# Kernel tuning notes

Measured on AMD Instinct MI355X. Metric: run time of the kernel, lower is better.

Reference implementation:

```python
import jax, jax.numpy as jnp
import numpy as np

N = 50000; E = 800000; F_IN = 128; H = 16; G = 256
DIMS = [F_IN, H, 2 * H, 4 * H, 4 * H, 8 * H]
EPS = 1e-5


def setup_inputs() -> dict:
    key = jax.random.key(0)
    ks = iter(jax.random.split(key, 40))
    inp = {}
    inp["x"] = jax.random.normal(next(ks), (N, F_IN), dtype=jnp.float32)
    inp["edge_index"] = jax.random.randint(next(ks), (2, E), 0, N, dtype=jnp.int32)
    inp["edge_weight"] = jax.random.uniform(next(ks), (E,), dtype=jnp.float32)
    inp["batch"] = jnp.sort(jax.random.randint(next(ks), (N,), 0, G, dtype=jnp.int32))
    for i in range(5):
        din, dout = DIMS[i], DIMS[i + 1]
        inp[f"W{i+1}"] = jax.random.normal(next(ks), (din, dout), dtype=jnp.float32) / np.sqrt(din).astype(np.float32)
        inp[f"b{i+1}"] = jnp.zeros((dout,), jnp.float32)
        inp[f"g{i+1}"] = jnp.ones((dout,), jnp.float32)
        inp[f"bt{i+1}"] = jnp.zeros((dout,), jnp.float32)
    inp["fc1_w"] = jax.random.normal(next(ks), (8 * H, 4 * H), dtype=jnp.float32) / np.sqrt(8 * H).astype(np.float32)
    inp["fc1_b"] = jnp.zeros((4 * H,), jnp.float32)
    inp["fc2_w"] = jax.random.normal(next(ks), (4 * H, 1), dtype=jnp.float32) / np.sqrt(4 * H).astype(np.float32)
    inp["fc2_b"] = jnp.zeros((1,), jnp.float32)
    return inp


def _gcn_norm(edge_index, edge_weight, n):
    # PyG GCNConv: add self-loops (weight 1), symmetric deg^-1/2 normalization.
    loop = jnp.arange(n, dtype=edge_index.dtype)
    row = jnp.concatenate([edge_index[0], loop])  # source
    col = jnp.concatenate([edge_index[1], loop])  # target
    w = jnp.concatenate([edge_weight, jnp.ones((n,), edge_weight.dtype)])
    deg = jax.ops.segment_sum(w, col, num_segments=n)
    dis = jnp.where(deg > 0, jax.lax.rsqrt(jnp.maximum(deg, 1e-12)), 0.0)
    return row, col, dis[row] * w * dis[col]


def _bn(h, g, b):
    # BatchNorm1d, training-mode batch statistics (biased variance, eps=1e-5)
    mu = h.mean(0)
    v = h.var(0)
    return g * (h - mu) * jax.lax.rsqrt(v + EPS) + b


def reference(x, edge_index, edge_weight, batch,
              W1, b1, g1, bt1, W2, b2, g2, bt2, W3, b3, g3, bt3,
              W4, b4, g4, bt4, W5, b5, g5, bt5,
              fc1_w, fc1_b, fc2_w, fc2_b):
    n = x.shape[0]
    row, col, norm = _gcn_norm(edge_index, edge_weight, n)

    def conv(h, W, b):
        m = h @ W                                   # [N, dout] dense transform
        agg = jax.ops.segment_sum(m[row] * norm[:, None], col, num_segments=n)
        return agg + b

    h = _bn(jax.nn.relu(conv(x, W1, b1)), g1, bt1)
    h = _bn(jax.nn.relu(conv(h, W2, b2)), g2, bt2)
    h = _bn(jax.nn.relu(conv(h, W3, b3)), g3, bt3)
    h = jax.nn.relu(_bn(conv(h, W4, b4), g4, bt4))   # layer4: conv->bn->relu
    h = _bn(conv(h, W5, b5), g5, bt5)                # layer5: conv->bn
    pooled = jax.ops.segment_sum(h, batch, num_segments=G)  # global_add_pool -> [G, 8H]
    p = jax.nn.relu(pooled)
    p = jax.nn.relu(p @ fc1_w + fc1_b)
    # dropout is identity in eval mode
    return (p @ fc2_w + fc2_b).reshape(-1)          # [G]
```

## Files before the change

kernel.cpp:

```cpp
#include <hip/hip_runtime.h>
#include <stdint.h>

#define NN 50000
#define NE 800000
#define NG 256
#define NBUCKET 16
#define PARTSZ (NBUCKET * 256)

#define NBKT 391
#define ABLK 391
#define ASLICE 2048
#define BCAP 2560

#define AFF4(u, sc, sh) { u.x = fmaxf(sc.x*u.x+sh.x,0.f); u.y = fmaxf(sc.y*u.y+sh.y,0.f); \
                          u.z = fmaxf(sc.z*u.z+sh.z,0.f); u.w = fmaxf(sc.w*u.w+sh.w,0.f); }

__device__ __forceinline__ void bn_coef(const double* __restrict__ partIn,
                                        const float* __restrict__ gmv,
                                        const float* __restrict__ btv,
                                        int tid, int n, float* scs, float* shs) {
    double s = 0., q = 0.;
#pragma unroll
    for (int b2 = 0; b2 < NBUCKET; ++b2) {
        s += partIn[b2 * 256 + tid];
        q += partIn[b2 * 256 + 128 + tid];
    }
    double mu = s / (double)n;
    double var = q / (double)n - mu * mu;
    float a = gmv[tid] * rsqrtf((float)var + 1e-5f);
    scs[tid] = a;
    shs[tid] = btv[tid] - (float)mu * a;
}

__device__ __forceinline__ void scan_totals(const int* __restrict__ totals,
                                            int* __restrict__ sbase, int tid) {
    if (tid < 64) {
        const int C = (NBKT + 63) / 64;
        int tv[C];
        int s = 0;
        int i0 = tid * C;
#pragma unroll
        for (int j = 0; j < C; ++j) {
            int idx = i0 + j;
            int x = (idx < NBKT) ? totals[idx] : 0;
            tv[j] = x; s += x;
        }
        int inc = s;
        for (int off = 1; off < 64; off <<= 1) {
            int t2 = __shfl_up(inc, off, 64);
            if (tid >= off) inc += t2;
        }
        int run = inc - s;
#pragma unroll
        for (int j = 0; j < C; ++j) {
            int idx = i0 + j;
            if (idx < NBKT) sbase[idx] = run;
            run += tv[j];
        }
        if (tid == 63) sbase[NBKT] = run;
    }
}

__global__ void kA1(const int* __restrict__ col, int* __restrict__ bb,
                    double* __restrict__ zz, int zn, int e) {
    __shared__ int cnt[NBKT];
    for (int j = threadIdx.x; j < NBKT; j += 256) cnt[j] = 0;
    for (int i = blockIdx.x * 256 + threadIdx.x; i < zn; i += ABLK * 256) zz[i] = 0.;
    __syncthreads();
    int start = blockIdx.x * ASLICE;
    int end = min(start + ASLICE, e);
    for (int i = start + threadIdx.x; i < end; i += 256)
        atomicAdd(&cnt[col[i] >> 7], 1);
    __syncthreads();
    for (int j = threadIdx.x; j < NBKT; j += 256) bb[blockIdx.x * NBKT + j] = cnt[j];
}

__global__ void kA2a(int* __restrict__ bb, int* __restrict__ totals) {
    __shared__ int v[ABLK];
    int k = blockIdx.x;
    int tid = threadIdx.x;
    for (int b = tid; b < ABLK; b += 256) v[b] = bb[b * NBKT + k];
    __syncthreads();
    if (tid < 64) {
        const int C = (ABLK + 63) / 64;
        int tv[C];
        int s = 0;
        int i0 = tid * C;
#pragma unroll
        for (int j = 0; j < C; ++j) {
            int idx = i0 + j;
            int x = (idx < ABLK) ? v[idx] : 0;
            tv[j] = x; s += x;
        }
        int inc = s;
        for (int off = 1; off < 64; off <<= 1) {
            int t2 = __shfl_up(inc, off, 64);
            if (tid >= off) inc += t2;
        }
        int run = inc - s;
#pragma unroll
        for (int j = 0; j < C; ++j) {
            int idx = i0 + j;
            if (idx < ABLK) v[idx] = run;
            run += tv[j];
        }
        if (tid == 63) totals[k] = run;
    }
    __syncthreads();
    for (int b = tid; b < ABLK; b += 256) bb[b * NBKT + k] = v[b];
}

__global__ void kA3g(const int* __restrict__ row, const int* __restrict__ col,
                     const float* __restrict__ ew, const int* __restrict__ bb,
                     const int* __restrict__ totals, int2* __restrict__ staging,
                     const float* __restrict__ x, const float* __restrict__ W0,
                     float* __restrict__ m1, int e, int n) {
    __shared__ int cur[NBKT];
    __shared__ int sbase[NBKT + 1];
    __shared__ float Wl[128 * 16];
    int tid = threadIdx.x;
    if ((int)blockIdx.x < ABLK) {
        scan_totals(totals, sbase, tid);
        __syncthreads();
        for (int j = tid; j < NBKT; j += 256)
            cur[j] = sbase[j] + bb[blockIdx.x * NBKT + j];
        __syncthreads();
        int start = blockIdx.x * ASLICE;
        int end = min(start + ASLICE, e);
        for (int i = start + tid; i < end; i += 256) {
            int c = col[i];
            int p = atomicAdd(&cur[c >> 7], 1);
            staging[p] = make_int2(row[i] | ((c & 127) << 16), __float_as_int(ew[i]));
        }
        return;
    }
    int bid = (int)blockIdx.x - ABLK;
    for (int i = tid; i < 128 * 16 / 4; i += 256)
        ((float4*)Wl)[i] = ((const float4*)W0)[i];
    __syncthreads();
    int jq = tid % 4, group = tid / 4;
    int node0 = (bid * 64 + group) * 2;
    const float4* h4 = (const float4*)x;
    int hb[2]; bool val[2];
#pragma unroll
    for (int i = 0; i < 2; ++i) {
        int nd = node0 + i;
        val[i] = nd < n;
        hb[i] = (val[i] ? nd : n - 1) * 32;
    }
    float4 acc[2];
    acc[0] = {0,0,0,0}; acc[1] = {0,0,0,0};
#pragma unroll 4
    for (int k4 = 0; k4 < 32; ++k4) {
        const float* wb = &Wl[(k4 * 4) * 16 + jq * 4];
        float4 w0 = *(const float4*)(wb);
        float4 w1 = *(const float4*)(wb + 16);
        float4 w2 = *(const float4*)(wb + 32);
        float4 w3 = *(const float4*)(wb + 48);
#pragma unroll
        for (int i = 0; i < 2; ++i) {
            float4 hv = h4[hb[i] + k4];
            acc[i].x += hv.x*w0.x + hv.y*w1.x + hv.z*w2.x + hv.w*w3.x;
            acc[i].y += hv.x*w0.y + hv.y*w1.y + hv.z*w2.y + hv.w*w3.y;
            acc[i].z += hv.x*w0.z + hv.y*w1.z + hv.z*w2.z + hv.w*w3.z;
            acc[i].w += hv.x*w0.w + hv.y*w1.w + hv.z*w2.w + hv.w*w3.w;
        }
    }
#pragma unroll
    for (int i = 0; i < 2; ++i)
        if (val[i]) ((float4*)m1)[(node0 + i) * 4 + jq] = acc[i];
}

__global__ void __launch_bounds__(256) kB(const int* __restrict__ totals,
                                          const int2* __restrict__ staging,
                                          int2* __restrict__ csr, int* __restrict__ ptr,
                                          float* __restrict__ dis, int n) {
    __shared__ int2 st[BCAP];
    __shared__ int2 outb[BCAP];
    __shared__ int hist[129];
    __shared__ int cur[128];
    __shared__ int sbase[NBKT + 1];
    int k = blockIdx.x, t = threadIdx.x;
    scan_totals(totals, sbase, t);
    if (t < 129) hist[t] = 0;
    __syncthreads();
    int base = sbase[k], cnt = sbase[k + 1] - sbase[k];
    int node0 = k << 7;
    int ncov = min(128, n - node0);
    if (cnt <= BCAP) {
        for (int i = t; i < cnt; i += 256) {
            int2 v = staging[base + i];
            st[i] = v;
            atomicAdd(&hist[v.x >> 16], 1);
        }
        __syncthreads();
        if (t == 0) {
            int run = 0;
            for (int j = 0; j < 128; ++j) { int h = hist[j]; hist[j] = run; run += h; }
            hist[128] = run;
        }
        __syncthreads();
        if (t < 128) cur[t] = hist[t];
        if (t < ncov) ptr[node0 + t] = base + hist[t];
        __syncthreads();
        for (int i = t; i < cnt; i += 256) {
            int2 v = st[i];
            int j = v.x >> 16;
            int p = atomicAdd(&cur[j], 1);
            outb[p] = make_int2(v.x & 0xFFFF, v.y);
        }
        __syncthreads();
        for (int i = t; i < cnt; i += 256) csr[base + i] = outb[i];
        if (t < ncov) {
            double s = 1.;
            int a = hist[t], b2 = hist[t + 1];
            for (int p = a; p < b2; ++p) s += (double)__int_as_float(outb[p].y);
            dis[node0 + t] = rsqrtf((float)s);
        }
    } else {
        for (int i = t; i < cnt; i += 256) atomicAdd(&hist[staging[base + i].x >> 16], 1);
        __syncthreads();
        if (t == 0) {
            int run = 0;
            for (int j = 0; j < 128; ++j) { int h = hist[j]; hist[j] = run; run += h; }
            hist[128] = run;
        }
        __syncthreads();
        if (t < 128) cur[t] = hist[t];
        if (t < ncov) ptr[node0 + t] = base + hist[t];
        __syncthreads();
        for (int i = t; i < cnt; i += 256) {
            int2 v = staging[base + i];
            int j = v.x >> 16;
            int p = atomicAdd(&cur[j], 1);
            csr[base + p] = make_int2(v.x & 0xFFFF, v.y);
        }
        __threadfence_block();
        __syncthreads();
        if (t < ncov) {
            double s = 1.;
            int a = hist[t], b2 = hist[t + 1];
            for (int p = a; p < b2; ++p) s += (double)__int_as_float(csr[base + p].y);
            dis[node0 + t] = rsqrtf((float)s);
        }
    }
    if (k == gridDim.x - 1 && t == 0) ptr[n] = sbase[NBKT];
}

__global__ void k_l1gather(const float* __restrict__ src, const int* __restrict__ ptr,
                           int2* __restrict__ csr, const float* __restrict__ dis,
                           const float* __restrict__ bias, double* __restrict__ partOut,
                           float* __restrict__ out, int n) {
    int tid = threadIdx.x;
    int t = blockIdx.x * 256 + tid;
    int node = t >> 2;
    int l4 = t & 3;
    bool valid = node < n;
    int nc = valid ? node : n - 1;
    const float4* s4 = (const float4*)src;
    float dc = dis[nc];
    float w0 = dc * dc;
    float4 v = s4[nc * 4 + l4];
    double ax = (double)(w0 * v.x), ay = (double)(w0 * v.y);
    double az = (double)(w0 * v.z), aw = (double)(w0 * v.w);
    int p0 = ptr[nc], p1 = ptr[nc + 1];
    int p = p0;
    for (; p + 4 <= p1; p += 4) {
        int2 c0 = csr[p], c1 = csr[p+1], c2 = csr[p+2], c3 = csr[p+3];
        float e0 = dis[c0.x] * __int_as_float(c0.y) * dc;
        float e1 = dis[c1.x] * __int_as_float(c1.y) * dc;
        float e2 = dis[c2.x] * __int_as_float(c2.y) * dc;
        float e3 = dis[c3.x] * __int_as_float(c3.y) * dc;
        float4 u0 = s4[c0.x * 4 + l4];
        float4 u1 = s4[c1.x * 4 + l4];
        float4 u2 = s4[c2.x * 4 + l4];
        float4 u3 = s4[c3.x * 4 + l4];
        ax += (double)(e0*u0.x) + (double)(e1*u1.x) + (double)(e2*u2.x) + (double)(e3*u3.x);
        ay += (double)(e0*u0.y) + (double)(e1*u1.y) + (double)(e2*u2.y) + (double)(e3*u3.y);
        az += (double)(e0*u0.z) + (double)(e1*u1.z) + (double)(e2*u2.z) + (double)(e3*u3.z);
        aw += (double)(e0*u0.w) + (double)(e1*u1.w) + (double)(e2*u2.w) + (double)(e3*u3.w);
        if (l4 == 0) {
            csr[p]   = make_int2(c0.x, __float_as_int(e0));
            csr[p+1] = make_int2(c1.x, __float_as_int(e1));
            csr[p+2] = make_int2(c2.x, __float_as_int(e2));
            csr[p+3] = make_int2(c3.x, __float_as_int(e3));
        }
    }
    for (; p < p1; ++p) {
        int2 ce = csr[p];
        float w = dis[ce.x] * __int_as_float(ce.y) * dc;
        float4 u = s4[ce.x * 4 + l4];
        ax += (double)(w*u.x); ay += (double)(w*u.y);
        az += (double)(w*u.z); aw += (double)(w*u.w);
        if (l4 == 0) csr[p] = make_int2(ce.x, __float_as_int(w));
    }
    float4 b = ((const float4*)bias)[l4];
    float4 acc;
    acc.x = fmaxf((float)ax + b.x, 0.f);
    acc.y = fmaxf((float)ay + b.y, 0.f);
    acc.z = fmaxf((float)az + b.z, 0.f);
    acc.w = fmaxf((float)aw + b.w, 0.f);
    if (valid) ((float4*)out)[nc * 4 + l4] = acc;
    float s0 = valid ? acc.x : 0.f, s1 = valid ? acc.y : 0.f;
    float s2 = valid ? acc.z : 0.f, s3 = valid ? acc.w : 0.f;
    float q0 = s0*s0, q1 = s1*s1, q2 = s2*s2, q3 = s3*s3;
    for (int off = 4; off < 64; off <<= 1) {
        s0 += __shfl_down(s0, off, 64); s1 += __shfl_down(s1, off, 64);
        s2 += __shfl_down(s2, off, 64); s3 += __shfl_down(s3, off, 64);
        q0 += __shfl_down(q0, off, 64); q1 += __shfl_down(q1, off, 64);
        q2 += __shfl_down(q2, off, 64); q3 += __shfl_down(q3, off, 64);
    }
    int lane = tid & 63;
    int bkt = (blockIdx.x & (NBUCKET - 1)) * 256;
    if (lane < 4) {
        atomicAdd(&partOut[bkt + 4*lane + 0], (double)s0);
        atomicAdd(&partOut[bkt + 4*lane + 1], (double)s1);
        atomicAdd(&partOut[bkt + 4*lane + 2], (double)s2);
        atomicAdd(&partOut[bkt + 4*lane + 3], (double)s3);
        atomicAdd(&partOut[bkt + 128 + 4*lane + 0], (double)q0);
        atomicAdd(&partOut[bkt + 128 + 4*lane + 1], (double)q1);
        atomicAdd(&partOut[bkt + 128 + 4*lane + 2], (double)q2);
        atomicAdd(&partOut[bkt + 128 + 4*lane + 3], (double)q3);
    }
}

template <int DIN, int DOUT, int EP, int POSTAFF, int RELU, int NPB>
__global__ void __launch_bounds__(256) k_fused(
        const float* __restrict__ src, const int* __restrict__ ptr,
        const int2* __restrict__ csr, const float* __restrict__ dis,
        const double* __restrict__ partIn, const float* __restrict__ gmv,
        const float* __restrict__ btv, const float* __restrict__ W,
        const float* __restrict__ bias, double* __restrict__ partOut,
        float* __restrict__ out, int n) {
    const int TPN1 = DIN / 4, LPN = TPN1 * EP, GN1 = 256 / LPN;
    const int TPN2 = DOUT / 4, G2 = 256 / TPN2;
    const int HS = DIN + 4;
    __shared__ float Wl[DIN * DOUT];
    __shared__ float hrow[NPB * HS];
    __shared__ float scs[DIN], shs[DIN];
    __shared__ double ls[DOUT], lq[DOUT];
    int tid = threadIdx.x;
    for (int i = tid; i < DIN * DOUT / 4; i += 256)
        ((float4*)Wl)[i] = ((const float4*)W)[i];
    if (tid < DIN) bn_coef(partIn, gmv, btv, tid, n, scs, shs);
    if (tid < DOUT) { ls[tid] = 0.; lq[tid] = 0.; }
    __syncthreads();

    int nodebase = blockIdx.x * NPB;
    {
        int grp = tid / LPN, r = tid % LPN;
        int e0 = r / TPN1, l4 = r % TPN1;
        float4 sc = ((const float4*)scs)[l4];
        float4 sh = ((const float4*)shs)[l4];
        const float4* s4 = (const float4*)src;
#pragma unroll
        for (int pass = 0; pass < NPB / GN1; ++pass) {
            int nl = pass * GN1 + grp;
            int node = nodebase + nl;
            int nc = node < n ? node : n - 1;
            double ax = 0., ay = 0., az = 0., aw = 0.;
            double sumw = 0.;
            if (e0 == 0) {
                float d = dis[nc];
                float w0 = d * d;
                float4 v = s4[(size_t)nc * TPN1 + l4];
                ax = (double)(w0*v.x); ay = (double)(w0*v.y);
                az = (double)(w0*v.z); aw = (double)(w0*v.w);
                sumw = (double)w0;
            }
            int p0 = ptr[nc], p1 = ptr[nc + 1];
            int p = p0 + e0;
            for (; p + 3 * EP < p1; p += 4 * EP) {
                int2 c0 = csr[p], c1 = csr[p + EP], c2 = csr[p + 2*EP], c3 = csr[p + 3*EP];
                float e0w = __int_as_float(c0.y), e1w = __int_as_float(c1.y);
                float e2w = __int_as_float(c2.y), e3w = __int_as_float(c3.y);
                float4 u0 = s4[(size_t)c0.x * TPN1 + l4];
                float4 u1 = s4[(size_t)c1.x * TPN1 + l4];
                float4 u2 = s4[(size_t)c2.x * TPN1 + l4];
                float4 u3 = s4[(size_t)c3.x * TPN1 + l4];
                ax += (double)(e0w*u0.x) + (double)(e1w*u1.x) + (double)(e2w*u2.x) + (double)(e3w*u3.x);
                ay += (double)(e0w*u0.y) + (double)(e1w*u1.y) + (double)(e2w*u2.y) + (double)(e3w*u3.y);
                az += (double)(e0w*u0.z) + (double)(e1w*u1.z) + (double)(e2w*u2.z) + (double)(e3w*u3.z);
                aw += (double)(e0w*u0.w) + (double)(e1w*u1.w) + (double)(e2w*u2.w) + (double)(e3w*u3.w);
                if (POSTAFF) sumw += (double)e0w + (double)e1w + (double)e2w + (double)e3w;
            }
            for (; p < p1; p += EP) {
                int2 ce = csr[p];
                float w = __int_as_float(ce.y);
                float4 u = s4[(size_t)ce.x * TPN1 + l4];
                ax += (double)(w*u.x); ay += (double)(w*u.y);
                az += (double)(w*u.z); aw += (double)(w*u.w);
                if (POSTAFF) sumw += (double)w;
            }
#pragma unroll
            for (int off = TPN1; off < LPN; off <<= 1) {
                ax += __shfl_xor(ax, off, 64);
                ay += __shfl_xor(ay, off, 64);
                az += __shfl_xor(az, off, 64);
                aw += __shfl_xor(aw, off, 64);
                if (POSTAFF) sumw += __shfl_xor(sumw, off, 64);
            }
            if (e0 == 0) {
                float4 acc;
                float sw = (float)sumw;
                acc.x = sc.x * (float)ax + sh.x * sw;
                acc.y = sc.y * (float)ay + sh.y * sw;
                acc.z = sc.z * (float)az + sh.z * sw;
                acc.w = sc.w * (float)aw + sh.w * sw;
                *(float4*)&hrow[nl * HS + (l4 << 2)] = acc;
            }
        }
    }
    __syncthreads();
    {
        int jq = tid % TPN2, g2 = tid / TPN2;
        float4 bv = ((const float4*)bias)[jq];
        float4 sv = {0,0,0,0}, qv = {0,0,0,0};
        for (int nl = g2; nl < NPB; nl += G2) {
            int node = nodebase + nl;
            bool valid = node < n;
            float4 a = {0.f, 0.f, 0.f, 0.f};
#pragma unroll
            for (int k4 = 0; k4 < DIN / 4; ++k4) {
                float4 hv = *(const float4*)&hrow[nl * HS + (k4 << 2)];
                const float* wb = &Wl[(k4 * 4) * DOUT + jq * 4];
                float4 w0 = *(const float4*)(wb);
                float4 w1 = *(const float4*)(wb + DOUT);
                float4 w2 = *(const float4*)(wb + 2 * DOUT);
                float4 w3 = *(const float4*)(wb + 3 * DOUT);
                a.x += hv.x*w0.x + hv.y*w1.x + hv.z*w2.x + hv.w*w3.x;
                a.y += hv.x*w0.y + hv.y*w1.y + hv.z*w2.y + hv.w*w3.y;
                a.z += hv.x*w0.z + hv.y*w1.z + hv.z*w2.z + hv.w*w3.z;
                a.w += hv.x*w0.w + hv.y*w1.w + hv.z*w2.w + hv.w*w3.w;
            }
            a.x += bv.x; a.y += bv.y; a.z += bv.z; a.w += bv.w;
            if (RELU) {
                a.x = fmaxf(a.x, 0.f); a.y = fmaxf(a.y, 0.f);
                a.z = fmaxf(a.z, 0.f); a.w = fmaxf(a.w, 0.f);
            }
            if (valid) {
                ((float4*)out)[(size_t)node * TPN2 + jq] = a;
                sv.x += a.x; sv.y += a.y; sv.z += a.z; sv.w += a.w;
                qv.x += a.x*a.x; qv.y += a.y*a.y; qv.z += a.z*a.z; qv.w += a.w*a.w;
            }
        }
        for (int off = TPN2; off < 64; off <<= 1) {
            sv.x += __shfl_down(sv.x, off, 64); sv.y += __shfl_down(sv.y, off, 64);
            sv.z += __shfl_down(sv.z, off, 64); sv.w += __shfl_down(sv.w, off, 64);
            qv.x += __shfl_down(qv.x, off, 64); qv.y += __shfl_down(qv.y, off, 64);
            qv.z += __shfl_down(qv.z, off, 64); qv.w += __shfl_down(qv.w, off, 64);
        }
        int lane = tid & 63;
        if (lane < TPN2) {
            atomicAdd(&ls[4*lane+0], (double)sv.x); atomicAdd(&ls[4*lane+1], (double)sv.y);
            atomicAdd(&ls[4*lane+2], (double)sv.z); atomicAdd(&ls[4*lane+3], (double)sv.w);
            atomicAdd(&lq[4*lane+0], (double)qv.x); atomicAdd(&lq[4*lane+1], (double)qv.y);
            atomicAdd(&lq[4*lane+2], (double)qv.z); atomicAdd(&lq[4*lane+3], (double)qv.w);
        }
        __syncthreads();
        int bkt = (blockIdx.x & (NBUCKET - 1)) * 256;
        if (tid < DOUT) {
            atomicAdd(&partOut[bkt + tid], ls[tid]);
            atomicAdd(&partOut[bkt + 128 + tid], lq[tid]);
        }
    }
}

template <int D, int POSTAFF, int PREAFF>
__global__ void __launch_bounds__(256) k_wgather(
        const float* __restrict__ src, const int* __restrict__ ptr,
        const int2* __restrict__ csr, const float* __restrict__ dis,
        const double* __restrict__ partIn, const float* __restrict__ gmv,
        const float* __restrict__ btv, float* __restrict__ out, int n) {
    const int RL = D / 4;
    const int EP = 4;
    const int LPN = RL * EP;
    __shared__ float scs[D], shs[D];
    int tid = threadIdx.x;
    if (tid < D) bn_coef(partIn, gmv, btv, tid, n, scs, shs);
    __syncthreads();
    int t = blockIdx.x * 256 + tid;
    int node = t / LPN;
    int r = t - node * LPN;
    int e0 = r / RL;
    int l4 = r - e0 * RL;
    bool valid = node < n;
    int nc = valid ? node : n - 1;
    const float4* s4 = (const float4*)src;
    float4 sc = ((const float4*)scs)[l4], sh = ((const float4*)shs)[l4];
    double ax = 0., ay = 0., az = 0., aw = 0.;
    double sumw = 0.;
    if (e0 == 0) {
        float d = dis[nc];
        float w0 = d * d;
        float4 v = s4[(size_t)nc * RL + l4];
        if (PREAFF) AFF4(v, sc, sh);
        ax = (double)(w0*v.x); ay = (double)(w0*v.y);
        az = (double)(w0*v.z); aw = (double)(w0*v.w);
        sumw = (double)w0;
    }
    int p0 = ptr[nc], p1 = ptr[nc + 1];
    int p = p0 + e0;
    for (; p + 3 * EP < p1; p += 4 * EP) {
        int2 c0 = csr[p], c1 = csr[p + EP], c2 = csr[p + 2*EP], c3 = csr[p + 3*EP];
        float w0 = __int_as_float(c0.y), w1 = __int_as_float(c1.y);
        float w2 = __int_as_float(c2.y), w3 = __int_as_float(c3.y);
        float4 u0 = s4[(size_t)c0.x * RL + l4];
        float4 u1 = s4[(size_t)c1.x * RL + l4];
        float4 u2 = s4[(size_t)c2.x * RL + l4];
        float4 u3 = s4[(size_t)c3.x * RL + l4];
        if (PREAFF) { AFF4(u0, sc, sh); AFF4(u1, sc, sh); AFF4(u2, sc, sh); AFF4(u3, sc, sh); }
        ax += (double)(w0*u0.x) + (double)(w1*u1.x) + (double)(w2*u2.x) + (double)(w3*u3.x);
        ay += (double)(w0*u0.y) + (double)(w1*u1.y) + (double)(w2*u2.y) + (double)(w3*u3.y);
        az += (double)(w0*u0.z) + (double)(w1*u1.z) + (double)(w2*u2.z) + (double)(w3*u3.z);
        aw += (double)(w0*u0.w) + (double)(w1*u1.w) + (double)(w2*u2.w) + (double)(w3*u3.w);
        if (POSTAFF) sumw += (double)w0 + (double)w1 + (double)w2 + (double)w3;
    }
    for (; p < p1; p += EP) {
        int2 ce = csr[p];
        float w = __int_as_float(ce.y);
        float4 u = s4[(size_t)ce.x * RL + l4];
        if (PREAFF) AFF4(u, sc, sh);
        ax += (double)(w*u.x); ay += (double)(w*u.y);
        az += (double)(w*u.z); aw += (double)(w*u.w);
        if (POSTAFF) sumw += (double)w;
    }
#pragma unroll
    for (int off = RL; off < LPN; off <<= 1) {
        ax += __shfl_xor(ax, off, 64); ay += __shfl_xor(ay, off, 64);
        az += __shfl_xor(az, off, 64); aw += __shfl_xor(aw, off, 64);
        if (POSTAFF) sumw += __shfl_xor(sumw, off, 64);
    }
    if (valid && e0 == 0) {
        float4 acc;
        if (POSTAFF) {
            float sw = (float)sumw;
            acc.x = sc.x * (float)ax + sh.x * sw;
            acc.y = sc.y * (float)ay + sh.y * sw;
            acc.z = sc.z * (float)az + sh.z * sw;
            acc.w = sc.w * (float)aw + sh.w * sw;
        } else {
            acc.x = (float)ax; acc.y = (float)ay;
            acc.z = (float)az; acc.w = (float)aw;
        }
        ((float4*)out)[(size_t)nc * RL + l4] = acc;
    }
}

template <int DIN, int DOUT, int RELU, int POOL>
__global__ void k_sgemm(const float* __restrict__ h, const float* __restrict__ W,
                        const float* __restrict__ bias, double* __restrict__ partOut,
                        float* __restrict__ m, const int* __restrict__ batch,
                        double* __restrict__ pooled, int n) {
    const int TPN = DOUT / 4, GPB = 256 / TPN, NPT = 4;
    const int NPBLK = GPB * NPT;
    const int MAXG = 34;
    __shared__ float Wl[DIN * DOUT];
    __shared__ double ls[DOUT], lq[DOUT];
    __shared__ double pool_l[POOL ? MAXG * DOUT : 1];
    __shared__ int gmaxs;
    int tid = threadIdx.x;
    for (int i = tid; i < DIN * DOUT / 4; i += 256)
        ((float4*)Wl)[i] = ((const float4*)W)[i];
    if (tid < DOUT) { ls[tid] = 0.; lq[tid] = 0.; }
    int gbase = 0;
    if (POOL) {
        for (int i = tid; i < MAXG * DOUT; i += 256) pool_l[i] = 0.;
        if (tid == 0) gmaxs = 0;
        int bn0 = blockIdx.x * NPBLK;
        gbase = batch[bn0 < n ? bn0 : n - 1];
    }
    __syncthreads();

    int jq = tid % TPN;
    int group = tid / TPN;
    int node0 = (blockIdx.x * GPB + group) * NPT;
    const float4* h4 = (const float4*)h;
    int hb[NPT]; bool val[NPT];
#pragma unroll
    for (int i = 0; i < NPT; ++i) {
        int nd = node0 + i;
        val[i] = nd < n;
        hb[i] = (val[i] ? nd : n - 1) * (DIN / 4);
    }
    float4 acc[NPT];
#pragma unroll
    for (int i = 0; i < NPT; ++i) acc[i] = {0.f, 0.f, 0.f, 0.f};
#pragma unroll 4
    for (int k4 = 0; k4 < DIN / 4; ++k4) {
        const float* wb = &Wl[(k4 * 4) * DOUT + jq * 4];
        float4 w0 = *(const float4*)(wb);
        float4 w1 = *(const float4*)(wb + DOUT);
        float4 w2 = *(const float4*)(wb + 2 * DOUT);
        float4 w3 = *(const float4*)(wb + 3 * DOUT);
#pragma unroll
        for (int i = 0; i < NPT; ++i) {
            float4 hv = h4[hb[i] + k4];
            acc[i].x += hv.x*w0.x + hv.y*w1.x + hv.z*w2.x + hv.w*w3.x;
            acc[i].y += hv.x*w0.y + hv.y*w1.y + hv.z*w2.y + hv.w*w3.y;
            acc[i].z += hv.x*w0.z + hv.y*w1.z + hv.z*w2.z + hv.w*w3.z;
            acc[i].w += hv.x*w0.w + hv.y*w1.w + hv.z*w2.w + hv.w*w3.w;
        }
    }
    float4 bv = ((const float4*)bias)[jq];
    float4 sv = {0,0,0,0}, qv = {0,0,0,0};
#pragma unroll
    for (int i = 0; i < NPT; ++i) {
        float4 a = acc[i];
        a.x += bv.x; a.y += bv.y; a.z += bv.z; a.w += bv.w;
        if (RELU) {
            a.x = fmaxf(a.x, 0.f); a.y = fmaxf(a.y, 0.f);
            a.z = fmaxf(a.z, 0.f); a.w = fmaxf(a.w, 0.f);
        }
        if (val[i]) {
            if (POOL) {
                int off = batch[node0 + i] - gbase;
                if (off < MAXG) {
                    atomicAdd(&pool_l[off * DOUT + jq * 4 + 0], (double)a.x);
                    atomicAdd(&pool_l[off * DOUT + jq * 4 + 1], (double)a.y);
                    atomicAdd(&pool_l[off * DOUT + jq * 4 + 2], (double)a.z);
                    atomicAdd(&pool_l[off * DOUT + jq * 4 + 3], (double)a.w);
                    if (jq == 0) atomicMax(&gmaxs, off);
                } else {
                    double* pg = &pooled[(size_t)(gbase + off) * DOUT + jq * 4];
                    atomicAdd(pg + 0, (double)a.x); atomicAdd(pg + 1, (double)a.y);
                    atomicAdd(pg + 2, (double)a.z); atomicAdd(pg + 3, (double)a.w);
                }
            } else {
                ((float4*)m)[(size_t)(node0 + i) * TPN + jq] = a;
            }
            sv.x += a.x; sv.y += a.y; sv.z += a.z; sv.w += a.w;
            qv.x += a.x*a.x; qv.y += a.y*a.y; qv.z += a.z*a.z; qv.w += a.w*a.w;
        }
    }
    for (int off = TPN; off < 64; off <<= 1) {
        sv.x += __shfl_down(sv.x, off, 64); sv.y += __shfl_down(sv.y, off, 64);
        sv.z += __shfl_down(sv.z, off, 64); sv.w += __shfl_down(sv.w, off, 64);
        qv.x += __shfl_down(qv.x, off, 64); qv.y += __shfl_down(qv.y, off, 64);
        qv.z += __shfl_down(qv.z, off, 64); qv.w += __shfl_down(qv.w, off, 64);
    }
    int lane = tid & 63;
    if (lane < TPN) {
        atomicAdd(&ls[4*lane+0], (double)sv.x); atomicAdd(&ls[4*lane+1], (double)sv.y);
        atomicAdd(&ls[4*lane+2], (double)sv.z); atomicAdd(&ls[4*lane+3], (double)sv.w);
        atomicAdd(&lq[4*lane+0], (double)qv.x); atomicAdd(&lq[4*lane+1], (double)qv.y);
        atomicAdd(&lq[4*lane+2], (double)qv.z); atomicAdd(&lq[4*lane+3], (double)qv.w);
    }
    __syncthreads();
    int bkt = (blockIdx.x & (NBUCKET - 1)) * 256;
    if (tid < DOUT) {
        atomicAdd(&partOut[bkt + tid], ls[tid]);
        atomicAdd(&partOut[bkt + 128 + tid], lq[tid]);
    }
    if (POOL) {
        int gm = gmaxs;
        for (int i = tid; i < (gm + 1) * DOUT; i += 256) {
            double v = pool_l[i];
            if (v != 0.) atomicAdd(&pooled[(size_t)gbase * DOUT + i], v);
        }
    }
}

__global__ void __launch_bounds__(128) k_poolhead(
        const double* __restrict__ pooled, const int* __restrict__ batch,
        const double* __restrict__ partIn, const float* __restrict__ gmv,
        const float* __restrict__ btv,
        const float* __restrict__ fc1w, const float* __restrict__ fc1b,
        const float* __restrict__ fc2w, const float* __restrict__ fc2b,
        float* __restrict__ out, int n) {
    __shared__ float pl[128];
    __shared__ float scs[128], shs[128];
    int g = blockIdx.x;
    int tid = threadIdx.x;
    bn_coef(partIn, gmv, btv, tid, n, scs, shs);
    int a = 0, b = n;
    while (a < b) { int mid = (a + b) >> 1; if (batch[mid] < g) a = mid + 1; else b = mid; }
    int lo = a;
    b = n;
    while (a < b) { int mid = (a + b) >> 1; if (batch[mid] < g + 1) a = mid + 1; else b = mid; }
    int hi = a;
    float cntf = (float)(hi - lo);
    float p = scs[tid] * (float)pooled[g * 128 + tid] + shs[tid] * cntf;
    pl[tid] = fmaxf(p, 0.f);
    __syncthreads();
    if (tid < 64) {
        float v1 = fc1b[tid];
        for (int k = 0; k < 128; ++k) v1 += pl[k] * fc1w[k * 64 + tid];
        v1 = fmaxf(v1, 0.f);
        float v = v1 * fc2w[tid];
        for (int off = 32; off > 0; off >>= 1) v += __shfl_down(v, off, 64);
        if (tid == 0) out[g] = v + fc2b[0];
    }
}

extern "C" void kernel_launch(void* const* d_in, const int* in_sizes, int n_in,
                              void* d_out, int out_size, void* d_ws, size_t ws_size,
                              hipStream_t stream) {
    const float* x     = (const float*)d_in[0];
    const int*   ei    = (const int*)d_in[1];
    const float* ew    = (const float*)d_in[2];
    const int*   batch = (const int*)d_in[3];
    const float *W[5], *b[5], *gm[5], *bt[5];
    for (int i = 0; i < 5; ++i) {
        W[i]  = (const float*)d_in[4 + 4 * i];
        b[i]  = (const float*)d_in[5 + 4 * i];
        gm[i] = (const float*)d_in[6 + 4 * i];
        bt[i] = (const float*)d_in[7 + 4 * i];
    }
    const float* fc1w = (const float*)d_in[24];
    const float* fc1b = (const float*)d_in[25];
    const float* fc2w = (const float*)d_in[26];
    const float* fc2b = (const float*)d_in[27];
    float* out = (float*)d_out;

    char* wsb = (char*)d_ws;
    float* dis    = (float*)wsb;  wsb += sizeof(float) * NN;
    int*   ptr    = (int*)wsb;    wsb += sizeof(int) * (NN + 4);
    int*   bb     = (int*)wsb;    wsb += sizeof(int) * ABLK * NBKT;
    int*   totals = (int*)wsb;    wsb += sizeof(int) * (NBKT + 1);
    wsb = (char*)(((uintptr_t)wsb + 15) & ~(uintptr_t)15);
    double* part   = (double*)wsb;  wsb += sizeof(double) * 5 * PARTSZ;
    double* pooled = (double*)wsb;  wsb += sizeof(double) * NG * 128;
    int2*  staging= (int2*)wsb;   wsb += sizeof(int2) * NE;
    int2*  csr    = (int2*)wsb;   wsb += sizeof(int2) * NE;
    float* bufB1  = (float*)wsb;  wsb += sizeof(float) * (size_t)NN * 64;
    float* bufB2  = (float*)wsb;  wsb += sizeof(float) * (size_t)NN * 64;
    float* buf1   = (float*)wsb;  wsb += sizeof(float) * (size_t)NN * 64;
    float* buf2   = (float*)wsb;  wsb += sizeof(float) * (size_t)NN * 16;

    const int* row = ei;
    const int* col = ei + NE;
    const int B = 256;
    const int NBF = (NN + 15) / 16;
    const int GB1 = (NN + 127) / 128;
    const int ZN = 5 * PARTSZ + NG * 128;

    kA1<<<ABLK, B, 0, stream>>>(col, bb, part, ZN, NE);
    kA2a<<<NBKT, B, 0, stream>>>(bb, totals);
    kA3g<<<ABLK + GB1, B, 0, stream>>>(row, col, ew, bb, totals, staging, x, W[0], buf1, NE, NN);
    kB<<<NBKT, B, 0, stream>>>(totals, staging, csr, ptr, dis, NN);

    k_l1gather<<<(NN * 4 + 255) / 256, B, 0, stream>>>(buf1, ptr, csr, dis,
                                                       b[0], part + 0 * PARTSZ, buf2, NN);

    k_fused<16, 32, 4, 1, 1, 16><<<NBF, B, 0, stream>>>(
        buf2, ptr, csr, dis, part + 0 * PARTSZ, gm[0], bt[0],
        W[1], b[1], part + 1 * PARTSZ, bufB1, NN);

    k_wgather<32, 1, 0><<<(int)(((long)NN * 32 + 255) / 256), B, 0, stream>>>(
        bufB1, ptr, csr, dis, part + 1 * PARTSZ, gm[1], bt[1], buf1, NN);
    k_sgemm<32, 64, 1, 0><<<(NN + 63) / 64, B, 0, stream>>>(
        buf1, W[2], b[2], part + 2 * PARTSZ, bufB2, nullptr, nullptr, NN);

    k_wgather<64, 1, 0><<<(int)(((long)NN * 64 + 255) / 256), B, 0, stream>>>(
        bufB2, ptr, csr, dis, part + 2 * PARTSZ, gm[2], bt[2], buf1, NN);
    k_sgemm<64, 64, 0, 0><<<(NN + 63) / 64, B, 0, stream>>>(
        buf1, W[3], b[3], part + 3 * PARTSZ, bufB1, nullptr, nullptr, NN);

    k_wgather<64, 0, 1><<<(int)(((long)NN * 64 + 255) / 256), B, 0, stream>>>(
        bufB1, ptr, csr, dis, part + 3 * PARTSZ, gm[3], bt[3], buf1, NN);
    k_sgemm<64, 128, 0, 1><<<(NN + 31) / 32, B, 0, stream>>>(
        buf1, W[4], b[4], part + 4 * PARTSZ, nullptr, batch, pooled, NN);

    k_poolhead<<<NG, 128, 0, stream>>>(pooled, batch, part + 4 * PARTSZ, gm[4], bt[4],
                                       fc1w, fc1b, fc2w, fc2b, out, NN);
}
```

Measured before the change: 382.6 us.

## Store gathered intermediate feature buffers in fp16 to halve gather traffic

The dense-transform outputs that feed the edge gathers (bufB1/bufB2) are now written as fp16 by k_fused and k_sgemm and read back as fp16 by k_wgather. Each gather thread now loads 8 halves with one 16-byte load instead of 4 floats, and the grid is halved to match. Accumulation stays in double. This is meant to cut the random-access memory traffic of the three edge gathers, which dominate the runtime, at the cost of fp16 rounding error in the intermediate activations.

Result: faster. 369.4 us (-3.4%).

```diff
diff --git a/kernel.cpp b/kernel.cpp
--- a/kernel.cpp
+++ b/kernel.cpp
@@ -1,4 +1,5 @@
 #include <hip/hip_runtime.h>
+#include <hip/hip_fp16.h>
 #include <stdint.h>
 
 #define NN 50000
@@ -11,6 +12,15 @@
 #define ABLK 391
 #define ASLICE 2048
 #define BCAP 2560
+
+__device__ __forceinline__ unsigned short f2h(float f) {
+    __half h = __float2half(f);
+    return *(unsigned short*)&h;
+}
+__device__ __forceinline__ float h2f(unsigned short u) {
+    __half h = *(__half*)&u;
+    return __half2float(h);
+}
 
 #define AFF4(u, sc, sh) { u.x = fmaxf(sc.x*u.x+sh.x,0.f); u.y = fmaxf(sc.y*u.y+sh.y,0.f); \
                           u.z = fmaxf(sc.z*u.z+sh.z,0.f); u.w = fmaxf(sc.w*u.w+sh.w,0.f); }
@@ -324,14 +334,24 @@
     }
 }
 
-template <int DIN, int DOUT, int EP, int POSTAFF, int RELU, int NPB>
+template <int D>
+__device__ __forceinline__ void ldrow16(const unsigned short* __restrict__ src, int node, int l8,
+                                        float4& a, float4& b) {
+    uint4 r = *(const uint4*)(src + (size_t)node * D + (l8 << 3));
+    a.x = h2f((unsigned short)(r.x)); a.y = h2f((unsigned short)(r.x >> 16));
+    a.z = h2f((unsigned short)(r.y)); a.w = h2f((unsigned short)(r.y >> 16));
+    b.x = h2f((unsigned short)(r.z)); b.y = h2f((unsigned short)(r.z >> 16));
+    b.z = h2f((unsigned short)(r.w)); b.w = h2f((unsigned short)(r.w >> 16));
+}
+
+template <int DIN, int DOUT, int EP, int RELU, int NPB>
 __global__ void __launch_bounds__(256) k_fused(
         const float* __restrict__ src, const int* __restrict__ ptr,
         const int2* __restrict__ csr, const float* __restrict__ dis,
         const double* __restrict__ partIn, const float* __restrict__ gmv,
         const float* __restrict__ btv, const float* __restrict__ W,
         const float* __restrict__ bias, double* __restrict__ partOut,
-        float* __restrict__ out, int n) {
+        unsigned short* __restrict__ out, int n) {
     const int TPN1 = DIN / 4, LPN = TPN1 * EP, GN1 = 256 / LPN;
     const int TPN2 = DOUT / 4, G2 = 256 / TPN2;
     const int HS = DIN + 4;
@@ -382,7 +402,7 @@
                 ay += (double)(e0w*u0.y) + (double)(e1w*u1.y) + (double)(e2w*u2.y) + (double)(e3w*u3.y);
                 az += (double)(e0w*u0.z) + (double)(e1w*u1.z) + (double)(e2w*u2.z) + (double)(e3w*u3.z);
                 aw += (double)(e0w*u0.w) + (double)(e1w*u1.w) + (double)(e2w*u2.w) + (double)(e3w*u3.w);
-                if (POSTAFF) sumw += (double)e0w + (double)e1w + (double)e2w + (double)e3w;
+                sumw += (double)e0w + (double)e1w + (double)e2w + (double)e3w;
             }
             for (; p < p1; p += EP) {
                 int2 ce = csr[p];
@@ -390,7 +410,7 @@
                 float4 u = s4[(size_t)ce.x * TPN1 + l4];
                 ax += (double)(w*u.x); ay += (double)(w*u.y);
                 az += (double)(w*u.z); aw += (double)(w*u.w);
-                if (POSTAFF) sumw += (double)w;
+                sumw += (double)w;
             }
 #pragma unroll
             for (int off = TPN1; off < LPN; off <<= 1) {
@@ -398,7 +418,7 @@
                 ay += __shfl_xor(ay, off, 64);
                 az += __shfl_xor(az, off, 64);
                 aw += __shfl_xor(aw, off, 64);
-                if (POSTAFF) sumw += __shfl_xor(sumw, off, 64);
+                sumw += __shfl_xor(sumw, off, 64);
             }
             if (e0 == 0) {
                 float4 acc;
@@ -439,7 +459,9 @@
                 a.z = fmaxf(a.z, 0.f); a.w = fmaxf(a.w, 0.f);
             }
             if (valid) {
-                ((float4*)out)[(size_t)node * TPN2 + jq] = a;
+                ushort4 o;
+                o.x = f2h(a.x); o.y = f2h(a.y); o.z = f2h(a.z); o.w = f2h(a.w);
+                *(ushort4*)(out + (size_t)node * DOUT + (jq << 2)) = o;
                 sv.x += a.x; sv.y += a.y; sv.z += a.z; sv.w += a.w;
                 qv.x += a.x*a.x; qv.y += a.y*a.y; qv.z += a.z*a.z; qv.w += a.w*a.w;
             }
@@ -468,11 +490,11 @@
 
 template <int D, int POSTAFF, int PREAFF>
 __global__ void __launch_bounds__(256) k_wgather(
-        const float* __restrict__ src, const int* __restrict__ ptr,
+        const unsigned short* __restrict__ src, const int* __restrict__ ptr,
         const int2* __restrict__ csr, const float* __restrict__ dis,
         const double* __restrict__ partIn, const float* __restrict__ gmv,
         const float* __restrict__ btv, float* __restrict__ out, int n) {
-    const int RL = D / 4;
+    const int RL = D / 8;
     const int EP = 4;
     const int LPN = RL * EP;
     __shared__ float scs[D], shs[D];
@@ -483,20 +505,24 @@
     int node = t / LPN;
     int r = t - node * LPN;
     int e0 = r / RL;
-    int l4 = r - e0 * RL;
+    int l8 = r - e0 * RL;
     bool valid = node < n;
     int nc = valid ? node : n - 1;
-    const float4* s4 = (const float4*)src;
-    float4 sc = ((const float4*)scs)[l4], sh = ((const float4*)shs)[l4];
-    double ax = 0., ay = 0., az = 0., aw = 0.;
+    float4 scA = ((const float4*)scs)[l8 * 2],     shA = ((const float4*)shs)[l8 * 2];
+    float4 scB = ((const float4*)scs)[l8 * 2 + 1], shB = ((const float4*)shs)[l8 * 2 + 1];
+    double aAx=0., aAy=0., aAz=0., aAw=0.;
+    double aBx=0., aBy=0., aBz=0., aBw=0.;
     double sumw = 0.;
     if (e0 == 0) {
         float d = dis[nc];
         float w0 = d * d;
-        float4 v = s4[(size_t)nc * RL + l4];
-        if (PREAFF) AFF4(v, sc, sh);
-        ax = (double)(w0*v.x); ay = (double)(w0*v.y);
-        az = (double)(w0*v.z); aw = (double)(w0*v.w);
+        float4 a, b2;
+        ldrow16<D>(src, nc, l8, a, b2);
+        if (PREAFF) { AFF4(a, scA, shA); AFF4(b2, scB, shB); }
+        aAx = (double)(w0*a.x);  aAy = (double)(w0*a.y);
+        aAz = (double)(w0*a.z);  aAw = (double)(w0*a.w);
+        aBx = (double)(w0*b2.x); aBy = (double)(w0*b2.y);
+        aBz = (double)(w0*b2.z); aBw = (double)(w0*b2.w);
         sumw = (double)w0;
     }
     int p0 = ptr[nc], p1 = ptr[nc + 1];
@@ -505,52 +531,74 @@
         int2 c0 = csr[p], c1 = csr[p + EP], c2 = csr[p + 2*EP], c3 = csr[p + 3*EP];
         float w0 = __int_as_float(c0.y), w1 = __int_as_float(c1.y);
         float w2 = __int_as_float(c2.y), w3 = __int_as_float(c3.y);
-        float4 u0 = s4[(size_t)c0.x * RL + l4];
-        float4 u1 = s4[(size_t)c1.x * RL + l4];
-        float4 u2 = s4[(size_t)c2.x * RL + l4];
-        float4 u3 = s4[(size_t)c3.x * RL + l4];
-        if (PREAFF) { AFF4(u0, sc, sh); AFF4(u1, sc, sh); AFF4(u2, sc, sh); AFF4(u3, sc, sh); }
-        ax += (double)(w0*u0.x) + (double)(w1*u1.x) + (double)(w2*u2.x) + (double)(w3*u3.x);
-        ay += (double)(w0*u0.y) + (double)(w1*u1.y) + (double)(w2*u2.y) + (double)(w3*u3.y);
-        az += (double)(w0*u0.z) + (double)(w1*u1.z) + (double)(w2*u2.z) + (double)(w3*u3.z);
-        aw += (double)(w0*u0.w) + (double)(w1*u1.w) + (double)(w2*u2.w) + (double)(w3*u3.w);
+        float4 a0, b0, a1, b1, a2, b2, a3, b3;
+        ldrow16<D>(src, c0.x, l8, a0, b0);
+        ldrow16<D>(src, c1.x, l8, a1, b1);
+        ldrow16<D>(src, c2.x, l8, a2, b2);
+        ldrow16<D>(src, c3.x, l8, a3, b3);
+        if (PREAFF) {
+            AFF4(a0, scA, shA); AFF4(b0, scB, shB);
+            AFF4(a1, scA, shA); AFF4(b1, scB, shB);
+            AFF4(a2, scA, shA); AFF4(b2, scB, shB);
+            AFF4(a3, scA, shA); AFF4(b3, scB, shB);
+        }
+        aAx += (double)(w0*a0.x) + (double)(w1*a1.x) + (double)(w2*a2.x) + (double)(w3*a3.x);
+        aAy += (double)(w0*a0.y) + (double)(w1*a1.y) + (double)(w2*a2.y) + (double)(w3*a3.y);
+        aAz += (double)(w0*a0.z) + (double)(w1*a1.z) + (double)(w2*a2.z) + (double)(w3*a3.z);
+        aAw += (double)(w0*a0.w) + (double)(w1*a1.w) + (double)(w2*a2.w) + (double)(w3*a3.w);
+        aBx += (double)(w0*b0.x) + (double)(w1*b1.x) + (double)(w2*b2.x) + (double)(w3*b3.x);
+        aBy += (double)(w0*b0.y) + (double)(w1*b1.y) + (double)(w2*b2.y) + (double)(w3*b3.y);
+        aBz += (double)(w0*b0.z) + (double)(w1*b1.z) + (double)(w2*b2.z) + (double)(w3*b3.z);
+        aBw += (double)(w0*b0.w) + (double)(w1*b1.w) + (double)(w2*b2.w) + (double)(w3*b3.w);
         if (POSTAFF) sumw += (double)w0 + (double)w1 + (double)w2 + (double)w3;
     }
     for (; p < p1; p += EP) {
         int2 ce = csr[p];
         float w = __int_as_float(ce.y);
-        float4 u = s4[(size_t)ce.x * RL + l4];
-        if (PREAFF) AFF4(u, sc, sh);
-        ax += (double)(w*u.x); ay += (double)(w*u.y);
-        az += (double)(w*u.z); aw += (double)(w*u.w);
+        float4 a, b2;
+        ldrow16<D>(src, ce.x, l8, a, b2);
+        if (PREAFF) { AFF4(a, scA, shA); AFF4(b2, scB, shB); }
+        aAx += (double)(w*a.x);  aAy += (double)(w*a.y);
+        aAz += (double)(w*a.z);  aAw += (double)(w*a.w);
+        aBx += (double)(w*b2.x); aBy += (double)(w*b2.y);
+        aBz += (double)(w*b2.z); aBw += (double)(w*b2.w);
         if (POSTAFF) sumw += (double)w;
     }
 #pragma unroll
     for (int off = RL; off < LPN; off <<= 1) {
-        ax += __shfl_xor(ax, off, 64); ay += __shfl_xor(ay, off, 64);
-        az += __shfl_xor(az, off, 64); aw += __shfl_xor(aw, off, 64);
+        aAx += __shfl_xor(aAx, off, 64); aAy += __shfl_xor(aAy, off, 64);
+        aAz += __shfl_xor(aAz, off, 64); aAw += __shfl_xor(aAw, off, 64);
+        aBx += __shfl_xor(aBx, off, 64); aBy += __shfl_xor(aBy, off, 64);
+        aBz += __shfl_xor(aBz, off, 64); aBw += __shfl_xor(aBw, off, 64);
         if (POSTAFF) sumw += __shfl_xor(sumw, off, 64);
     }
     if (valid && e0 == 0) {
-        float4 acc;
+        float4 accA, accB;
         if (POSTAFF) {
             float sw = (float)sumw;
-            acc.x = sc.x * (float)ax + sh.x * sw;
-            acc.y = sc.y * (float)ay + sh.y * sw;
-            acc.z = sc.z * (float)az + sh.z * sw;
-            acc.w = sc.w * (float)aw + sh.w * sw;
+            accA.x = scA.x * (float)aAx + shA.x * sw;
+            accA.y = scA.y * (float)aAy + shA.y * sw;
+            accA.z = scA.z * (float)aAz + shA.z * sw;
+            accA.w = scA.w * (float)aAw + shA.w * sw;
+            accB.x = scB.x * (float)aBx + shB.x * sw;
+            accB.y = scB.y * (float)aBy + shB.y * sw;
+            accB.z = scB.z * (float)aBz + shB.z * sw;
+            accB.w = scB.w * (float)aBw + shB.w * sw;
         } else {
-            acc.x = (float)ax; acc.y = (float)ay;
-            acc.z = (float)az; acc.w = (float)aw;
-        }
-        ((float4*)out)[(size_t)nc * RL + l4] = acc;
-    }
-}
-
-template <int DIN, int DOUT, int RELU, int POOL>
+            accA.x = (float)aAx; accA.y = (float)aAy;
+            accA.z = (float)aAz; accA.w = (float)aAw;
+            accB.x = (float)aBx; accB.y = (float)aBy;
+            accB.z = (float)aBz; accB.w = (float)aBw;
+        }
+        ((float4*)out)[(size_t)nc * (D / 4) + l8 * 2]     = accA;
+        ((float4*)out)[(size_t)nc * (D / 4) + l8 * 2 + 1] = accB;
+    }
+}
+
+template <int DIN, int DOUT, int RELU, int F16OUT, int POOL>
 __global__ void k_sgemm(const float* __restrict__ h, const float* __restrict__ W,
                         const float* __restrict__ bias, double* __restrict__ partOut,
-                        float* __restrict__ m, const int* __restrict__ batch,
+                        void* __restrict__ m, const int* __restrict__ batch,
                         double* __restrict__ pooled, int n) {
     const int TPN = DOUT / 4, GPB = 256 / TPN, NPT = 4;
     const int NPBLK = GPB * NPT;
@@ -626,6 +674,10 @@
                     atomicAdd(pg + 0, (double)a.x); atomicAdd(pg + 1, (double)a.y);
                     atomicAdd(pg + 2, (double)a.z); atomicAdd(pg + 3, (double)a.w);
                 }
+            } else if (F16OUT) {
+                ushort4 o;
+                o.x = f2h(a.x); o.y = f2h(a.y); o.z = f2h(a.z); o.w = f2h(a.w);
+                *(ushort4*)((unsigned short*)m + (size_t)(node0 + i) * DOUT + (jq << 2)) = o;
             } else {
                 ((float4*)m)[(size_t)(node0 + i) * TPN + jq] = a;
             }
@@ -723,8 +775,8 @@
     double* pooled = (double*)wsb;  wsb += sizeof(double) * NG * 128;
     int2*  staging= (int2*)wsb;   wsb += sizeof(int2) * NE;
     int2*  csr    = (int2*)wsb;   wsb += sizeof(int2) * NE;
-    float* bufB1  = (float*)wsb;  wsb += sizeof(float) * (size_t)NN * 64;
-    float* bufB2  = (float*)wsb;  wsb += sizeof(float) * (size_t)NN * 64;
+    unsigned short* bufB1h = (unsigned short*)wsb; wsb += sizeof(unsigned short) * (size_t)NN * 64;
+    unsigned short* bufB2h = (unsigned short*)wsb; wsb += sizeof(unsigned short) * (size_t)NN * 64;
     float* buf1   = (float*)wsb;  wsb += sizeof(float) * (size_t)NN * 64;
     float* buf2   = (float*)wsb;  wsb += sizeof(float) * (size_t)NN * 16;
 
@@ -743,23 +795,23 @@
     k_l1gather<<<(NN * 4 + 255) / 256, B, 0, stream>>>(buf1, ptr, csr, dis,
                                                        b[0], part + 0 * PARTSZ, buf2, NN);
 
-    k_fused<16, 32, 4, 1, 1, 16><<<NBF, B, 0, stream>>>(
+    k_fused<16, 32, 4, 1, 16><<<NBF, B, 0, stream>>>(
         buf2, ptr, csr, dis, part + 0 * PARTSZ, gm[0], bt[0],
-        W[1], b[1], part + 1 * PARTSZ, bufB1, NN);
-
-    k_wgather<32, 1, 0><<<(int)(((long)NN * 32 + 255) / 256), B, 0, stream>>>(
-        bufB1, ptr, csr, dis, part + 1 * PARTSZ, gm[1], bt[1], buf1, NN);
-    k_sgemm<32, 64, 1, 0><<<(NN + 63) / 64, B, 0, stream>>>(
-        buf1, W[2], b[2], part + 2 * PARTSZ, bufB2, nullptr, nullptr, NN);
-
-    k_wgather<64, 1, 0><<<(int)(((long)NN * 64 + 255) / 256), B, 0, stream>>>(
-        bufB2, ptr, csr, dis, part + 2 * PARTSZ, gm[2], bt[2], buf1, NN);
-    k_sgemm<64, 64, 0, 0><<<(NN + 63) / 64, B, 0, stream>>>(
-        buf1, W[3], b[3], part + 3 * PARTSZ, bufB1, nullptr, nullptr, NN);
-
-    k_wgather<64, 0, 1><<<(int)(((long)NN * 64 + 255) / 256), B, 0, stream>>>(
-        bufB1, ptr, csr, dis, part + 3 * PARTSZ, gm[3], bt[3], buf1, NN);
-    k_sgemm<64, 128, 0, 1><<<(NN + 31) / 32, B, 0, stream>>>(
+        W[1], b[1], part + 1 * PARTSZ, bufB1h, NN);
+
+    k_wgather<32, 1, 0><<<(int)(((long)NN * 16 + 255) / 256), B, 0, stream>>>(
+        bufB1h, ptr, csr, dis, part + 1 * PARTSZ, gm[1], bt[1], buf1, NN);
+    k_sgemm<32, 64, 1, 1, 0><<<(NN + 63) / 64, B, 0, stream>>>(
+        buf1, W[2], b[2], part + 2 * PARTSZ, bufB2h, nullptr, nullptr, NN);
+
+    k_wgather<64, 1, 0><<<(int)(((long)NN * 32 + 255) / 256), B, 0, stream>>>(
+        bufB2h, ptr, csr, dis, part + 2 * PARTSZ, gm[2], bt[2], buf1, NN);
+    k_sgemm<64, 64, 0, 1, 0><<<(NN + 63) / 64, B, 0, stream>>>(
+        buf1, W[3], b[3], part + 3 * PARTSZ, bufB1h, nullptr, nullptr, NN);
+
+    k_wgather<64, 0, 1><<<(int)(((long)NN * 32 + 255) / 256), B, 0, stream>>>(
+        bufB1h, ptr, csr, dis, part + 3 * PARTSZ, gm[3], bt[3], buf1, NN);
+    k_sgemm<64, 128, 0, 0, 1><<<(NN + 31) / 32, B, 0, stream>>>(
         buf1, W[4], b[4], part + 4 * PARTSZ, nullptr, batch, pooled, NN);
 
     k_poolhead<<<NG, 128, 0, stream>>>(pooled, batch, part + 4 * PARTSZ, gm[4], bt[4],
```
